# Kernel tuning notes

Hardware: AMD Instinct MI355X
Metric: run time of the kernel (lower is better)

## Reference

```python
import jax, jax.numpy as jnp
import numpy as np
import math

B, S, D, H = 4, 1024, 1024, 16
DK = D // H
HID = 2 * D
EPS = 1e-5

def _lin(key, din, dout):
    kw, kb = jax.random.split(key)
    sc = 1.0 / math.sqrt(din)
    return (jax.random.uniform(kw, (din, dout), jnp.float32, -sc, sc),
            jax.random.uniform(kb, (dout,), jnp.float32, -sc, sc))

def setup_inputs() -> dict:
    key = jax.random.key(0)
    ks = jax.random.split(key, 10)
    x = jax.random.normal(ks[0], (B, S, D), jnp.float32)
    y = jax.random.normal(ks[1], (B, S, D), jnp.float32)
    # additive causal mask (zeros below/on diag, -1e9 above)
    mask = jnp.where(jnp.tril(jnp.ones((S, S), bool)), 0.0, -1e9).astype(jnp.float32)
    qkv_w, qkv_b = _lin(ks[2], D, 3 * D)
    ao_w, ao_b = _lin(ks[3], D, D)
    kv_w, kv_b = _lin(ks[4], D, 2 * D)
    q_w, q_b = _lin(ks[5], D, D)
    co_w, co_b = _lin(ks[6], D, D)
    fc1_w, fc1_b = _lin(ks[7], D, HID)
    fc2_w, fc2_b = _lin(ks[8], HID, D)
    g = jnp.ones((D,), jnp.float32)
    b = jnp.zeros((D,), jnp.float32)
    return dict(x=x, y=y, mask=mask,
                qkv_w=qkv_w, qkv_b=qkv_b, ao_w=ao_w, ao_b=ao_b,
                kv_w=kv_w, kv_b=kv_b, q_w=q_w, q_b=q_b, co_w=co_w, co_b=co_b,
                fc1_w=fc1_w, fc1_b=fc1_b, fc2_w=fc2_w, fc2_b=fc2_b,
                ln1_g=g, ln1_b=b, ln2_g=g, ln2_b=b, ln3_g=g, ln3_b=b)

def _heads(t):  # [B,S,D] -> [B,H,S,DK]
    return t.reshape(B, S, H, -1).transpose(0, 2, 1, 3)

def _merge(t):  # [B,H,S,DK] -> [B,S,D]
    return t.transpose(0, 2, 1, 3).reshape(B, S, D)

def _attn(q, k, v, mask):
    scores = jnp.einsum('bhqd,bhkd->bhqk', q, k) / math.sqrt(q.shape[-1])
    if mask is not None:
        scores = scores + mask
    p = jax.nn.softmax(scores, axis=-1)
    return jnp.einsum('bhqk,bhkd->bhqd', p, v)

def _ln(t, g, b):
    mu = jnp.mean(t, axis=-1, keepdims=True)
    var = jnp.mean(jnp.square(t - mu), axis=-1, keepdims=True)
    return (t - mu) / jnp.sqrt(var + EPS) * g + b

def reference(x, y, mask, qkv_w, qkv_b, ao_w, ao_b, kv_w, kv_b, q_w, q_b,
              co_w, co_b, fc1_w, fc1_b, fc2_w, fc2_b,
              ln1_g, ln1_b, ln2_g, ln2_b, ln3_g, ln3_b):
    # masked self-attention on y
    qkv = y @ qkv_w + qkv_b
    qh, kh, vh = jnp.split(_heads(qkv), 3, axis=-1)
    sa = _merge(_attn(qh, kh, vh, mask)) @ ao_w + ao_b
    y_att = _ln(sa + y, ln1_g, ln1_b)  # dropout is identity (eval)
    # cross-attention: kv from x, q from ORIGINAL y (as in source), no mask
    kv = _heads(x @ kv_w + kv_b)
    ck, cv = jnp.split(kv, 2, axis=-1)
    cq = _heads(y @ q_w + q_b)
    cross = _merge(_attn(cq, ck, cv, None)) @ co_w + co_b
    # quirk in source: LN applied BEFORE residual add here
    y_cross = _ln(cross, ln2_g, ln2_b) + y_att
    # feedforward (hidden = 2*d_model)
    ff = jax.nn.relu(y_cross @ fc1_w + fc1_b) @ fc2_w + fc2_b
    return _ln(ff + y_cross, ln3_g, ln3_b)
```

## Files before the change

### kernel.cpp

```cpp
#include <hip/hip_runtime.h>
#include <cstdint>
#include <cstddef>


#define DEV __device__ __forceinline__

typedef __bf16 bf16x8 __attribute__((ext_vector_type(8)));
typedef float f32x4 __attribute__((ext_vector_type(4)));

DEV float bf2f(uint16_t h) { return __builtin_bit_cast(float, (uint32_t)h << 16); }
DEV uint16_t f2bf(float f) {
  uint32_t u = __builtin_bit_cast(uint32_t, f);
  return (uint16_t)((u + 0x7fffu + ((u >> 16) & 1u)) >> 16);
}

DEV void gload16(const void* g, void* l) {
  __builtin_amdgcn_global_load_lds((const __attribute__((address_space(1))) void*)g,
                                   (__attribute__((address_space(3))) void*)l, 16, 0, 0);
}

__global__ __launch_bounds__(256) void prep(
    const float* __restrict__ x, const float* __restrict__ y,
    uint16_t* __restrict__ xb, uint16_t* __restrict__ yb,
    const float* __restrict__ w0, uint16_t* __restrict__ t0,
    const float* __restrict__ w1, uint16_t* __restrict__ t1,
    const float* __restrict__ w2, uint16_t* __restrict__ t2,
    const float* __restrict__ w3, uint16_t* __restrict__ t3,
    const float* __restrict__ w4, uint16_t* __restrict__ t4,
    const float* __restrict__ w5, uint16_t* __restrict__ t5,
    const float* __restrict__ w6, uint16_t* __restrict__ t6) {
  int bid = blockIdx.x;
  const int tid = threadIdx.x;
  if (bid < 8192) {
    const float* src = (bid < 4096) ? x : y;
    uint16_t* dst = (bid < 4096) ? xb : yb;
    const int i = (bid & 4095) * 256 + tid;
    const float4 v = ((const float4*)src)[i];
    const uint32_t lo = (uint32_t)f2bf(v.x) | ((uint32_t)f2bf(v.y) << 16);
    const uint32_t hi = (uint32_t)f2bf(v.z) | ((uint32_t)f2bf(v.w) << 16);
    ((uint2*)dst)[i] = make_uint2(lo, hi);
    return;
  }
  bid -= 8192;
  const float* W; uint16_t* T; int K, N, tile;
  if (bid < 3072)       { W = w0; T = t0; K = 1024; N = 3072; tile = bid; }
  else if (bid < 4096)  { W = w1; T = t1; K = 1024; N = 1024; tile = bid - 3072; }
  else if (bid < 6144)  { W = w2; T = t2; K = 1024; N = 2048; tile = bid - 4096; }
  else if (bid < 7168)  { W = w3; T = t3; K = 1024; N = 1024; tile = bid - 6144; }
  else if (bid < 8192)  { W = w4; T = t4; K = 1024; N = 1024; tile = bid - 7168; }
  else if (bid < 10240) { W = w5; T = t5; K = 1024; N = 2048; tile = bid - 8192; }
  else                  { W = w6; T = t6; K = 2048; N = 1024; tile = bid - 10240; }
  const int ntx = N >> 5;
  const int n0 = (tile % ntx) * 32, k0 = (tile / ntx) * 32;
  __shared__ float t[32][33];
  const int tx = tid & 31, ty = tid >> 5;
#pragma unroll
  for (int i = 0; i < 32; i += 8)
    t[ty + i][tx] = W[(size_t)(k0 + ty + i) * N + n0 + tx];
  __syncthreads();
#pragma unroll
  for (int i = 0; i < 32; i += 8)
    T[(size_t)(n0 + ty + i) * K + k0 + tx] = f2bf(t[tx][ty + i]);
}

enum { EP_QKV = 0, EP_RES_F32RES, EP_SCKV, EP_Q, EP_F32, EP_RELU, EP_RES_B16RES };

template <int EPI>
__global__ __launch_bounds__(256) void gemm_bt(const uint16_t* __restrict__ A,
                                               const uint16_t* __restrict__ Bt,
                                               const float* __restrict__ bias,
                                               void* __restrict__ out0,
                                               const void* __restrict__ res,
                                               int M, int N, int K) {
  __shared__ __align__(16) uint16_t As[128 * 32];
  __shared__ __align__(16) uint16_t Bs[128 * 32];
  const int tid = threadIdx.x;
  const int wid = tid >> 6, lane = tid & 63;
  const int g = lane >> 4, lr = lane & 15;
  const int wr = wid >> 1, wc = wid & 1;
  const int m0 = blockIdx.y * 128, n0 = blockIdx.x * 128;

  const char* Ab = (const char*)A;
  const char* Bb = (const char*)Bt;
  const size_t rs = (size_t)K * 2;

  const int rc = lane >> 2;
  const int scb = ((lane & 3) << 4) ^ ((rc & 3) << 4);

  int aoff[4], boff[4];
#pragma unroll
  for (int m = 0; m < 4; ++m) {
    const int row = wr * 64 + m * 16 + lr;
    aoff[m] = row * 64 + ((g * 16) ^ ((row & 3) << 4));
  }
#pragma unroll
  for (int n = 0; n < 4; ++n) {
    const int row = wc * 64 + n * 16 + lr;
    boff[n] = row * 64 + ((g * 16) ^ ((row & 3) << 4));
  }

  f32x4 acc[4][4] = {};
  const int nk = K >> 5;
  for (int kt = 0; kt < nk; ++kt) {
    __syncthreads();
#pragma unroll
    for (int i = 0; i < 2; ++i) {
      const int c = wid * 2 + i;
      gload16(Ab + (size_t)(m0 + c * 16 + rc) * rs + (size_t)kt * 64 + scb,
              (void*)((char*)As + c * 1024));
      gload16(Bb + (size_t)(n0 + c * 16 + rc) * rs + (size_t)kt * 64 + scb,
              (void*)((char*)Bs + c * 1024));
    }
    asm volatile("s_waitcnt vmcnt(0)" ::: "memory");
    __syncthreads();

    bf16x8 av[4], bv[4];
#pragma unroll
    for (int m = 0; m < 4; ++m) av[m] = *(const bf16x8*)((const char*)As + aoff[m]);
#pragma unroll
    for (int n = 0; n < 4; ++n) bv[n] = *(const bf16x8*)((const char*)Bs + boff[n]);
#pragma unroll
    for (int m = 0; m < 4; ++m)
#pragma unroll
      for (int n = 0; n < 4; ++n)
        acc[m][n] = __builtin_amdgcn_mfma_f32_16x16x32_bf16(av[m], bv[n], acc[m][n], 0, 0, 0);
  }

#pragma unroll
  for (int m = 0; m < 4; ++m) {
#pragma unroll
    for (int n = 0; n < 4; ++n) {
      const int gcol = n0 + wc * 64 + n * 16 + lr;
      const float bb = bias[gcol];
#pragma unroll
      for (int r = 0; r < 4; ++r) {
        const int grow = m0 + wr * 64 + m * 16 + g * 4 + r;
        float v = acc[m][n][r] + bb;
        if constexpr (EPI == EP_QKV) {
          const int b = grow >> 10, s = grow & 1023;
          const int h = gcol / 192;
          const int rr = gcol - h * 192;
          const int part = rr >> 6, d = rr & 63;
          const int bh = b * 16 + h;
          uint16_t* base = (uint16_t*)out0;
          if (part == 2)
            base[2u * 4194304u + ((size_t)bh * 64 + d) * 1024 + s] = f2bf(v);
          else
            base[(size_t)part * 4194304u + ((size_t)bh * 1024 + s) * 64 + d] = f2bf(v);
        } else if constexpr (EPI == EP_SCKV) {
          const int b = grow >> 10, s = grow & 1023;
          const int h = gcol >> 7, part = (gcol >> 6) & 1, d = gcol & 63;
          const int bh = b * 16 + h;
          uint16_t* base = (uint16_t*)out0;
          if (part == 0)
            base[((size_t)bh * 1024 + s) * 64 + d] = f2bf(v);
          else
            base[4194304u + ((size_t)bh * 64 + d) * 1024 + s] = f2bf(v);
        } else if constexpr (EPI == EP_Q) {
          const int b = grow >> 10, s = grow & 1023;
          const int h = gcol >> 6, d = gcol & 63;
          ((uint16_t*)out0)[((size_t)(b * 16 + h) * 1024 + s) * 64 + d] = f2bf(v);
        } else if constexpr (EPI == EP_RES_F32RES) {
          v += ((const float*)res)[(size_t)grow * N + gcol];
          ((float*)out0)[(size_t)grow * N + gcol] = v;
        } else if constexpr (EPI == EP_F32) {
          ((float*)out0)[(size_t)grow * N + gcol] = v;
        } else if constexpr (EPI == EP_RELU) {
          ((uint16_t*)out0)[(size_t)grow * N + gcol] = f2bf(v > 0.f ? v : 0.f);
        } else if constexpr (EPI == EP_RES_B16RES) {
          v += bf2f(((const uint16_t*)res)[(size_t)grow * N + gcol]);
          ((float*)out0)[(size_t)grow * N + gcol] = v;
        }
      }
    }
  }
}

template <bool CAUSAL>
__global__ __launch_bounds__(256) void attn_fused(const uint16_t* __restrict__ Qp,
                                                  const uint16_t* __restrict__ Kp,
                                                  const uint16_t* __restrict__ Vtp,
                                                  uint16_t* __restrict__ O) {
  __shared__ __align__(16) uint16_t Kl[2][64 * 64];
  __shared__ __align__(16) uint16_t Vl[2][64 * 64];
  __shared__ __align__(16) uint16_t Pl[4][16 * 64];
  const int tid = threadIdx.x, wid = tid >> 6, lane = tid & 63;
  const int g = lane >> 4, lr = lane & 15;
  const int qb = blockIdx.x, bh = blockIdx.y;
  const char* Qb = (const char*)(Qp + (size_t)bh * 65536);
  const char* Kb = (const char*)(Kp + (size_t)bh * 65536);
  const char* Vb = (const char*)(Vtp + (size_t)bh * 65536);
  const int q0 = qb * 64 + wid * 16;

  bf16x8 aq[2];
#pragma unroll
  for (int ks = 0; ks < 2; ++ks)
    aq[ks] = *(const bf16x8*)(Qb + ((size_t)(q0 + lr) * 64 + ks * 32 + g * 8) * 2);

  float m_run[4], l_run[4];
  f32x4 oacc[4] = {};
#pragma unroll
  for (int r = 0; r < 4; ++r) { m_run[r] = -1e30f; l_run[r] = 0.f; }

  const int rc = lane >> 3;
  const int scb = ((lane & 7) << 4) ^ (rc << 4);
  const int nkt = CAUSAL ? (qb + 1) : 16;
  char* Pb = (char*)Pl[wid];

  auto stage = [&](int kt, int bufi) {
#pragma unroll
    for (int i = 0; i < 2; ++i) {
      const int c = wid * 2 + i;
      gload16(Kb + (size_t)(kt * 64 + c * 8 + rc) * 128 + scb,
              (void*)((char*)Kl[bufi] + c * 1024));
      gload16(Vb + (size_t)(c * 8 + rc) * 2048 + kt * 128 + scb,
              (void*)((char*)Vl[bufi] + c * 1024));
    }
  };

  stage(0, 0);
  asm volatile("s_waitcnt vmcnt(0)" ::: "memory");
  __syncthreads();

  for (int kt = 0; kt < nkt; ++kt) {
    const int cur = kt & 1;
    if (kt + 1 < nkt) stage(kt + 1, cur ^ 1);
    const char* Kc = (const char*)Kl[cur];
    const char* Vc = (const char*)Vl[cur];
    const int nlim = (CAUSAL && kt == qb) ? wid : 3;

    f32x4 sc[4];
#pragma unroll
    for (int n = 0; n < 4; ++n) {
      if (n <= nlim) {
        f32x4 t = {};
#pragma unroll
        for (int ks = 0; ks < 2; ++ks) {
          const int row = n * 16 + lr;
          bf16x8 bk = *(const bf16x8*)(Kc + row * 128 + ((ks * 64 + g * 16) ^ ((row & 7) << 4)));
          t = __builtin_amdgcn_mfma_f32_16x16x32_bf16(aq[ks], bk, t, 0, 0, 0);
        }
        sc[n] = t;
      } else {
        sc[n] = f32x4{-1e10f, -1e10f, -1e10f, -1e10f};
      }
    }

    float p[4][4];
#pragma unroll
    for (int n = 0; n < 4; ++n)
#pragma unroll
      for (int r = 0; r < 4; ++r) {
        float v = sc[n][r] * 0.125f;
        if (CAUSAL) {
          const int k_abs = kt * 64 + n * 16 + lr;
          const int q_abs = q0 + g * 4 + r;
          if (k_abs > q_abs) v = -1e9f;
        }
        p[n][r] = v;
      }
#pragma unroll
    for (int r = 0; r < 4; ++r) {
      float mx = fmaxf(fmaxf(p[0][r], p[1][r]), fmaxf(p[2][r], p[3][r]));
      mx = fmaxf(mx, __shfl_xor(mx, 1));
      mx = fmaxf(mx, __shfl_xor(mx, 2));
      mx = fmaxf(mx, __shfl_xor(mx, 4));
      mx = fmaxf(mx, __shfl_xor(mx, 8));
      const float mnew = fmaxf(m_run[r], mx);
      const float f = __expf(m_run[r] - mnew);
      m_run[r] = mnew;
      float ls = 0.f;
#pragma unroll
      for (int n = 0; n < 4; ++n) {
        const float e = __expf(p[n][r] - mnew);
        p[n][r] = e;
        ls += e;
      }
      ls += __shfl_xor(ls, 1);
      ls += __shfl_xor(ls, 2);
      ls += __shfl_xor(ls, 4);
      ls += __shfl_xor(ls, 8);
      l_run[r] = l_run[r] * f + ls;
#pragma unroll
      for (int n = 0; n < 4; ++n) oacc[n][r] *= f;
    }
#pragma unroll
    for (int n = 0; n < 4; ++n)
#pragma unroll
      for (int r = 0; r < 4; ++r) {
        const int row = g * 4 + r;
        *(uint16_t*)(Pb + row * 128 + ((n * 32 + lr * 2) ^ ((row & 7) << 4))) = f2bf(p[n][r]);
      }
    asm volatile("s_waitcnt lgkmcnt(0)" ::: "memory");
#pragma unroll
    for (int ks = 0; ks < 2; ++ks) {
      bf16x8 pa = *(const bf16x8*)(Pb + lr * 128 + ((ks * 64 + g * 16) ^ ((lr & 7) << 4)));
#pragma unroll
      for (int n2 = 0; n2 < 4; ++n2) {
        const int row = n2 * 16 + lr;
        bf16x8 bv = *(const bf16x8*)(Vc + row * 128 + ((ks * 64 + g * 16) ^ ((row & 7) << 4)));
        oacc[n2] = __builtin_amdgcn_mfma_f32_16x16x32_bf16(pa, bv, oacc[n2], 0, 0, 0);
      }
    }
    asm volatile("s_waitcnt vmcnt(0)" ::: "memory");
    __syncthreads();
  }

  const int b = bh >> 4, h = bh & 15;
#pragma unroll
  for (int n2 = 0; n2 < 4; ++n2)
#pragma unroll
    for (int r = 0; r < 4; ++r) {
      const int q = q0 + g * 4 + r, d = n2 * 16 + lr;
      const float v = oacc[n2][r] / l_run[r];
      O[(size_t)(b * 1024 + q) * 1024 + h * 64 + d] = f2bf(v);
    }
}

__global__ __launch_bounds__(256) void ln_kernel(const float* __restrict__ in,
                                                 const float* __restrict__ gam,
                                                 const float* __restrict__ bet,
                                                 const float* __restrict__ addend,
                                                 float* __restrict__ outf,
                                                 uint16_t* __restrict__ outb) {
  __shared__ float red[4];
  const int tid = threadIdx.x;
  const size_t row = blockIdx.x;
  const float4 v = ((const float4*)(in + row * 1024))[tid];
  float s = v.x + v.y + v.z + v.w;
#pragma unroll
  for (int o = 1; o < 64; o <<= 1) s += __shfl_xor(s, o);
  const int wid = tid >> 6, lane = tid & 63;
  if (lane == 0) red[wid] = s;
  __syncthreads();
  s = red[0] + red[1] + red[2] + red[3];
  const float mu = s * (1.f / 1024.f);
  const float d0 = v.x - mu, d1 = v.y - mu, d2 = v.z - mu, d3 = v.w - mu;
  float sq = d0 * d0 + d1 * d1 + d2 * d2 + d3 * d3;
  __syncthreads();
#pragma unroll
  for (int o = 1; o < 64; o <<= 1) sq += __shfl_xor(sq, o);
  if (lane == 0) red[wid] = sq;
  __syncthreads();
  sq = red[0] + red[1] + red[2] + red[3];
  const float inv = rsqrtf(sq * (1.f / 1024.f) + 1e-5f);
  const float4 gv = ((const float4*)(gam))[tid];
  const float4 bv = ((const float4*)(bet))[tid];
  float o0 = d0 * inv * gv.x + bv.x;
  float o1 = d1 * inv * gv.y + bv.y;
  float o2 = d2 * inv * gv.z + bv.z;
  float o3 = d3 * inv * gv.w + bv.w;
  if (addend) {
    const float4 a = ((const float4*)(addend + row * 1024))[tid];
    o0 += a.x; o1 += a.y; o2 += a.z; o3 += a.w;
  }
  if (outf)
    ((float4*)(outf + row * 1024))[tid] = make_float4(o0, o1, o2, o3);
  if (outb) {
    const uint32_t w0 = (uint32_t)f2bf(o0) | ((uint32_t)f2bf(o1) << 16);
    const uint32_t w1 = (uint32_t)f2bf(o2) | ((uint32_t)f2bf(o3) << 16);
    ((uint2*)(outb + row * 1024))[tid] = make_uint2(w0, w1);
  }
}

extern "C" void kernel_launch(void* const* d_in, const int* in_sizes, int n_in,
                              void* d_out, int out_size, void* d_ws, size_t ws_size,
                              hipStream_t stream) {
  (void)in_sizes; (void)n_in; (void)out_size; (void)ws_size;
  const float* x     = (const float*)d_in[0];
  const float* y     = (const float*)d_in[1];
  const float* qkv_w = (const float*)d_in[3];
  const float* qkv_b = (const float*)d_in[4];
  const float* ao_w  = (const float*)d_in[5];
  const float* ao_b  = (const float*)d_in[6];
  const float* kv_w  = (const float*)d_in[7];
  const float* kv_b  = (const float*)d_in[8];
  const float* q_w   = (const float*)d_in[9];
  const float* q_b   = (const float*)d_in[10];
  const float* co_w  = (const float*)d_in[11];
  const float* co_b  = (const float*)d_in[12];
  const float* fc1_w = (const float*)d_in[13];
  const float* fc1_b = (const float*)d_in[14];
  const float* fc2_w = (const float*)d_in[15];
  const float* fc2_b = (const float*)d_in[16];
  const float* ln1_g = (const float*)d_in[17];
  const float* ln1_b = (const float*)d_in[18];
  const float* ln2_g = (const float*)d_in[19];
  const float* ln2_b = (const float*)d_in[20];
  const float* ln3_g = (const float*)d_in[21];
  const float* ln3_b = (const float*)d_in[22];

  char* ws = (char*)d_ws;
  size_t off = 0;
  auto alloc = [&](size_t bytes) {
    char* p = ws + off;
    off += (bytes + 255) & ~(size_t)255;
    return p;
  };
  uint16_t* xb     = (uint16_t*)alloc(4194304ull * 2);
  uint16_t* yb     = (uint16_t*)alloc(4194304ull * 2);
  uint16_t* wT_qkv = (uint16_t*)alloc(3072ull * 1024 * 2);
  uint16_t* wT_ao  = (uint16_t*)alloc(1024ull * 1024 * 2);
  uint16_t* wT_kv  = (uint16_t*)alloc(2048ull * 1024 * 2);
  uint16_t* wT_q   = (uint16_t*)alloc(1024ull * 1024 * 2);
  uint16_t* wT_co  = (uint16_t*)alloc(1024ull * 1024 * 2);
  uint16_t* wT_fc1 = (uint16_t*)alloc(2048ull * 1024 * 2);
  uint16_t* wT_fc2 = (uint16_t*)alloc(1024ull * 2048 * 2);
  uint16_t* QKV    = (uint16_t*)alloc(3ull * 4194304 * 2);
  uint16_t* SA     = (uint16_t*)alloc(4194304ull * 2);
  float*    YATT   = (float*)alloc(4194304ull * 4);
  float*    TMP    = (float*)alloc(4194304ull * 4);
  uint16_t* YCB    = (uint16_t*)alloc(4194304ull * 2);

  const dim3 blk(256);

  prep<<<dim3(20480), blk, 0, stream>>>(x, y, xb, yb,
                                        qkv_w, wT_qkv, ao_w, wT_ao, kv_w, wT_kv,
                                        q_w, wT_q, co_w, wT_co, fc1_w, wT_fc1, fc2_w, wT_fc2);

  gemm_bt<EP_QKV><<<dim3(24, 32), blk, 0, stream>>>(yb, wT_qkv, qkv_b, QKV, nullptr, 4096, 3072, 1024);
  attn_fused<true><<<dim3(16, 64), blk, 0, stream>>>(QKV, QKV + 4194304, QKV + 2 * 4194304, SA);
  gemm_bt<EP_RES_F32RES><<<dim3(8, 32), blk, 0, stream>>>(SA, wT_ao, ao_b, TMP, y, 4096, 1024, 1024);
  ln_kernel<<<dim3(4096), blk, 0, stream>>>(TMP, ln1_g, ln1_b, nullptr, YATT, nullptr);
  gemm_bt<EP_SCKV><<<dim3(16, 32), blk, 0, stream>>>(xb, wT_kv, kv_b, QKV + 4194304, nullptr, 4096, 2048, 1024);
  gemm_bt<EP_Q><<<dim3(8, 32), blk, 0, stream>>>(yb, wT_q, q_b, QKV, nullptr, 4096, 1024, 1024);
  attn_fused<false><<<dim3(16, 64), blk, 0, stream>>>(QKV, QKV + 4194304, QKV + 2 * 4194304, SA);
  gemm_bt<EP_F32><<<dim3(8, 32), blk, 0, stream>>>(SA, wT_co, co_b, TMP, nullptr, 4096, 1024, 1024);
  ln_kernel<<<dim3(4096), blk, 0, stream>>>(TMP, ln2_g, ln2_b, YATT, nullptr, YCB);
  gemm_bt<EP_RELU><<<dim3(16, 32), blk, 0, stream>>>(YCB, wT_fc1, fc1_b, (uint16_t*)YATT, nullptr, 4096, 2048, 1024);
  gemm_bt<EP_RES_B16RES><<<dim3(8, 32), blk, 0, stream>>>((const uint16_t*)YATT, wT_fc2, fc2_b, TMP, YCB, 4096, 1024, 2048);
  ln_kernel<<<dim3(4096), blk, 0, stream>>>(TMP, ln3_g, ln3_b, nullptr, (float*)d_out, nullptr);
}
```

Baseline: 542.4 us.

## Transpose score MFMA, use exp2 softmax, and balance causal block order

The QK^T MFMA operands are swapped so each lane holds one query row's scores. Row max and sum then need only two cross-lane shuffles instead of four per row, and P is written to LDS as packed 64-bit stores. The softmax scale is folded into a log2(e) factor so exp2f replaces __expf. Causal query blocks are interleaved short/long so that long and short rows are paired across the grid, which should improve load balance. In exchange, the rescale factors and the final normaliser now need extra shuffles to reach the O accumulator layout.

```diff
diff --git a/kernel.cpp b/kernel.cpp
--- a/kernel.cpp
+++ b/kernel.cpp
@@ -186,21 +186,21 @@
   __shared__ __align__(16) uint16_t Pl[4][16 * 64];
   const int tid = threadIdx.x, wid = tid >> 6, lane = tid & 63;
   const int g = lane >> 4, lr = lane & 15;
-  const int qb = blockIdx.x, bh = blockIdx.y;
+  const int qbx = blockIdx.x, bh = blockIdx.y;
+  const int qb = CAUSAL ? ((qbx & 1) ? (15 - (qbx >> 1)) : (qbx >> 1)) : qbx;
   const char* Qb = (const char*)(Qp + (size_t)bh * 65536);
   const char* Kb = (const char*)(Kp + (size_t)bh * 65536);
   const char* Vb = (const char*)(Vtp + (size_t)bh * 65536);
   const int q0 = qb * 64 + wid * 16;
+  const float SCALE = 0.18033688011112042f;
 
   bf16x8 aq[2];
 #pragma unroll
   for (int ks = 0; ks < 2; ++ks)
     aq[ks] = *(const bf16x8*)(Qb + ((size_t)(q0 + lr) * 64 + ks * 32 + g * 8) * 2);
 
-  float m_run[4], l_run[4];
+  float m_run = -1e30f, l_run = 0.f;
   f32x4 oacc[4] = {};
-#pragma unroll
-  for (int r = 0; r < 4; ++r) { m_run[r] = -1e30f; l_run[r] = 0.f; }
 
   const int rc = lane >> 3;
   const int scb = ((lane & 7) << 4) ^ (rc << 4);
@@ -229,7 +229,7 @@
     const char* Vc = (const char*)Vl[cur];
     const int nlim = (CAUSAL && kt == qb) ? wid : 3;
 
-    f32x4 sc[4];
+    float p[4][4];
 #pragma unroll
     for (int n = 0; n < 4; ++n) {
       if (n <= nlim) {
@@ -238,59 +238,60 @@
         for (int ks = 0; ks < 2; ++ks) {
           const int row = n * 16 + lr;
           bf16x8 bk = *(const bf16x8*)(Kc + row * 128 + ((ks * 64 + g * 16) ^ ((row & 7) << 4)));
-          t = __builtin_amdgcn_mfma_f32_16x16x32_bf16(aq[ks], bk, t, 0, 0, 0);
+          t = __builtin_amdgcn_mfma_f32_16x16x32_bf16(bk, aq[ks], t, 0, 0, 0);
         }
-        sc[n] = t;
+#pragma unroll
+        for (int r = 0; r < 4; ++r) p[n][r] = t[r] * SCALE;
       } else {
-        sc[n] = f32x4{-1e10f, -1e10f, -1e10f, -1e10f};
+#pragma unroll
+        for (int r = 0; r < 4; ++r) p[n][r] = -1e9f;
       }
     }
-
-    float p[4][4];
+    if (CAUSAL && kt == qb) {
+      const int q_abs = q0 + lr;
+#pragma unroll
+      for (int n = 0; n < 4; ++n)
+#pragma unroll
+        for (int r = 0; r < 4; ++r)
+          if (kt * 64 + n * 16 + g * 4 + r > q_abs) p[n][r] = -1e9f;
+    }
+
+    float mx = -1e30f;
 #pragma unroll
     for (int n = 0; n < 4; ++n)
 #pragma unroll
+      for (int r = 0; r < 4; ++r) mx = fmaxf(mx, p[n][r]);
+    mx = fmaxf(mx, __shfl_xor(mx, 16));
+    mx = fmaxf(mx, __shfl_xor(mx, 32));
+    const float mnew = fmaxf(m_run, mx);
+    const float f = exp2f(m_run - mnew);
+    m_run = mnew;
+    float ls = 0.f;
+#pragma unroll
+    for (int n = 0; n < 4; ++n)
+#pragma unroll
       for (int r = 0; r < 4; ++r) {
-        float v = sc[n][r] * 0.125f;
-        if (CAUSAL) {
-          const int k_abs = kt * 64 + n * 16 + lr;
-          const int q_abs = q0 + g * 4 + r;
-          if (k_abs > q_abs) v = -1e9f;
-        }
-        p[n][r] = v;
-      }
-#pragma unroll
-    for (int r = 0; r < 4; ++r) {
-      float mx = fmaxf(fmaxf(p[0][r], p[1][r]), fmaxf(p[2][r], p[3][r]));
-      mx = fmaxf(mx, __shfl_xor(mx, 1));
-      mx = fmaxf(mx, __shfl_xor(mx, 2));
-      mx = fmaxf(mx, __shfl_xor(mx, 4));
-      mx = fmaxf(mx, __shfl_xor(mx, 8));
-      const float mnew = fmaxf(m_run[r], mx);
-      const float f = __expf(m_run[r] - mnew);
-      m_run[r] = mnew;
-      float ls = 0.f;
-#pragma unroll
-      for (int n = 0; n < 4; ++n) {
-        const float e = __expf(p[n][r] - mnew);
+        const float e = exp2f(p[n][r] - mnew);
         p[n][r] = e;
         ls += e;
       }
-      ls += __shfl_xor(ls, 1);
-      ls += __shfl_xor(ls, 2);
-      ls += __shfl_xor(ls, 4);
-      ls += __shfl_xor(ls, 8);
-      l_run[r] = l_run[r] * f + ls;
-#pragma unroll
-      for (int n = 0; n < 4; ++n) oacc[n][r] *= f;
-    }
-#pragma unroll
-    for (int n = 0; n < 4; ++n)
-#pragma unroll
-      for (int r = 0; r < 4; ++r) {
-        const int row = g * 4 + r;
-        *(uint16_t*)(Pb + row * 128 + ((n * 32 + lr * 2) ^ ((row & 7) << 4))) = f2bf(p[n][r]);
-      }
+    ls += __shfl_xor(ls, 16);
+    ls += __shfl_xor(ls, 32);
+    l_run = l_run * f + ls;
+    float fb[4];
+#pragma unroll
+    for (int r = 0; r < 4; ++r) fb[r] = __shfl(f, g * 4 + r);
+#pragma unroll
+    for (int n2 = 0; n2 < 4; ++n2)
+#pragma unroll
+      for (int r = 0; r < 4; ++r) oacc[n2][r] *= fb[r];
+
+#pragma unroll
+    for (int n = 0; n < 4; ++n) {
+      const uint32_t w0 = (uint32_t)f2bf(p[n][0]) | ((uint32_t)f2bf(p[n][1]) << 16);
+      const uint32_t w1 = (uint32_t)f2bf(p[n][2]) | ((uint32_t)f2bf(p[n][3]) << 16);
+      *(uint2*)(Pb + lr * 128 + ((n * 32 + g * 8) ^ ((lr & 7) << 4))) = make_uint2(w0, w1);
+    }
     asm volatile("s_waitcnt lgkmcnt(0)" ::: "memory");
 #pragma unroll
     for (int ks = 0; ks < 2; ++ks) {
@@ -306,13 +307,16 @@
     __syncthreads();
   }
 
+  float lb[4];
+#pragma unroll
+  for (int r = 0; r < 4; ++r) lb[r] = __shfl(l_run, g * 4 + r);
   const int b = bh >> 4, h = bh & 15;
 #pragma unroll
   for (int n2 = 0; n2 < 4; ++n2)
 #pragma unroll
     for (int r = 0; r < 4; ++r) {
       const int q = q0 + g * 4 + r, d = n2 * 16 + lr;
-      const float v = oacc[n2][r] / l_run[r];
+      const float v = oacc[n2][r] / lb[r];
       O[(size_t)(b * 1024 + q) * 1024 + h * 64 + d] = f2bf(v);
     }
 }
```

After: 512.2 us. 1.06x faster.
